# Optimization experiments

Measured on AMD Instinct MI355X. Metric: run time of the kernel, lower is better.

Reference implementation:

```python
import math
import jax, jax.numpy as jnp
import numpy as np

B = 128          # graphs per batch
N = 1024         # nodes per graph
E = 1048576      # total edges (avg degree 8)
F_IN = 64
NHID = 64
NCLS = 10
RATIO = 0.8


def setup_inputs() -> dict:
    key = jax.random.key(0)
    ks = jax.random.split(key, 24)
    x = jax.random.normal(ks[0], (B * N, F_IN), jnp.float32)
    # intra-graph random edges: graph id per edge, local src/dst
    epg = E // B
    gid = jnp.repeat(jnp.arange(B, dtype=jnp.int32), epg)
    src = gid * N + jax.random.randint(ks[1], (E,), 0, N, jnp.int32)
    dst = gid * N + jax.random.randint(ks[2], (E,), 0, N, jnp.int32)
    def lin(k, fi, fo):
        s = 1.0 / np.sqrt(fi)
        return jax.random.uniform(k, (fi, fo), jnp.float32, -s, s)
    p = {
        'W1': lin(ks[3], F_IN, NHID), 'b1': jnp.zeros((NHID,), jnp.float32),
        'Wp1': lin(ks[4], NHID, 1), 'bp1': jnp.zeros((1,), jnp.float32),
        'W2': lin(ks[5], NHID, NHID), 'b2': jnp.zeros((NHID,), jnp.float32),
        'Wp2': lin(ks[6], NHID, 1), 'bp2': jnp.zeros((1,), jnp.float32),
        'W3': lin(ks[7], NHID, NHID), 'b3': jnp.zeros((NHID,), jnp.float32),
        'Wp3': lin(ks[8], NHID, 1), 'bp3': jnp.zeros((1,), jnp.float32),
        'L1w': lin(ks[9], 2 * NHID, NHID), 'L1b': jnp.zeros((NHID,), jnp.float32),
        'L2w': lin(ks[10], NHID, NHID // 2), 'L2b': jnp.zeros((NHID // 2,), jnp.float32),
        'L3w': lin(ks[11], NHID // 2, NCLS), 'L3b': jnp.zeros((NCLS,), jnp.float32),
    }
    return dict(x=x, edge_src=src, edge_dst=dst, **p)


def gcn_conv(x, W, b, src, dst, emask, n):
    # PyG GCNConv: add self loops, symmetric deg normalization
    xw = x @ W
    ew = emask.astype(x.dtype)
    deg = jax.ops.segment_sum(ew, dst, num_segments=n) + 1.0  # +1 self loop
    dis = jax.lax.rsqrt(deg)
    norm = dis[src] * dis[dst] * ew
    agg = jax.ops.segment_sum(xw[src] * norm[:, None], dst, num_segments=n)
    agg = agg + xw * (dis * dis)[:, None]  # self-loop message
    return agg + b


def sag_pool(x, Wp, bp, src, dst, emask, n_cur):
    n_tot = B * n_cur
    k = int(math.ceil(RATIO * n_cur))
    score = gcn_conv(x, Wp, bp, src, dst, emask, n_tot)[:, 0]
    _, idx = jax.lax.top_k(score.reshape(B, n_cur), k)
    perm = (idx + (jnp.arange(B, dtype=jnp.int32) * n_cur)[:, None]).reshape(-1)
    xn = x[perm] * jnp.tanh(score[perm])[:, None]
    new_idx = jnp.full((n_tot,), -1, jnp.int32).at[perm].set(
        jnp.arange(B * k, dtype=jnp.int32))
    ns, nd = new_idx[src], new_idx[dst]
    valid = emask & (ns >= 0) & (nd >= 0)
    return xn, jnp.where(valid, ns, 0), jnp.where(valid, nd, 0), valid, k


def readout(x, k):
    xr = x.reshape(B, k, NHID)
    return jnp.concatenate([xr.max(axis=1), xr.mean(axis=1)], axis=1)


def reference(x, edge_src, edge_dst, W1, b1, Wp1, bp1, W2, b2, Wp2, bp2,
              W3, b3, Wp3, bp3, L1w, L1b, L2w, L2b, L3w, L3b):
    src = edge_src.astype(jnp.int32)
    dst = edge_dst.astype(jnp.int32)
    emask = jnp.ones((E,), bool)
    n = N
    h = jax.nn.relu(gcn_conv(x, W1, b1, src, dst, emask, B * n))
    h, src, dst, emask, n = sag_pool(h, Wp1, bp1, src, dst, emask, n)
    r1 = readout(h, n)
    h = jax.nn.relu(gcn_conv(h, W2, b2, src, dst, emask, B * n))
    h, src, dst, emask, n = sag_pool(h, Wp2, bp2, src, dst, emask, n)
    r2 = readout(h, n)
    h = jax.nn.relu(gcn_conv(h, W3, b3, src, dst, emask, B * n))
    h, src, dst, emask, n = sag_pool(h, Wp3, bp3, src, dst, emask, n)
    r3 = readout(h, n)
    z = r1 + r2 + r3
    z = jax.nn.relu(z @ L1w + L1b)          # dropout is identity in eval
    z = jax.nn.relu(z @ L2w + L2b)
    return jax.nn.log_softmax(z @ L3w + L3b, axis=-1)
```

## Files before the change

kernel.cpp:

```cpp
#include <hip/hip_runtime.h>
#include <math.h>

constexpr int B_  = 128;
constexpr int N_  = 1024;
constexpr int E_  = 1048576;
constexpr int BN_ = B_ * N_;
constexpr int EPG = E_ / B_;
constexpr int NSEG = 16;

typedef short v8s __attribute__((ext_vector_type(8)));
typedef float v4f __attribute__((ext_vector_type(4)));

__device__ __forceinline__ unsigned bf16_rne(unsigned u) {
    return (u + 0x7FFFu + ((u >> 16) & 1u)) >> 16;
}

__global__ __launch_bounds__(1024) void k_csr2(
        const int* __restrict__ src, const int* __restrict__ dst,
        const int* __restrict__ cum,
        int* __restrict__ srt, int* __restrict__ rowptr,
        float* __restrict__ dis, int n) {
    __shared__ int cnt[1024];
    __shared__ int cur[1024];
    __shared__ int cums[1024];
    __shared__ int wsum[17];
    int g = blockIdx.x, tid = threadIdx.x;
    int gb   = g * N_;
    int base = g * n;
    const int eb = g * EPG;

    cums[tid] = cum ? cum[gb + tid] : tid;
    cnt[tid] = 0;
    __syncthreads();
    for (int t = tid; t < EPG; t += 1024) {
        int s = cums[src[eb + t] - gb];
        int d = cums[dst[eb + t] - gb];
        if ((s | d) >= 0) atomicAdd(&cnt[d], 1);
    }
    __syncthreads();

    int c = (tid < n) ? cnt[tid] : 0;
    int v = c;
    int lane = tid & 63, wv = tid >> 6;
    #pragma unroll
    for (int off = 1; off < 64; off <<= 1) {
        int t = __shfl_up(v, off, 64);
        if (lane >= off) v += t;
    }
    if (lane == 63) wsum[wv] = v;
    __syncthreads();
    if (tid == 0) {
        int run = 0;
        #pragma unroll
        for (int i = 0; i < 16; ++i) { int t = wsum[i]; wsum[i] = run; run += t; }
        wsum[16] = run;
    }
    __syncthreads();
    int excl = v - c + wsum[wv];
    if (tid < n) {
        cur[tid] = excl;
        rowptr[g * (n + 1) + tid] = excl;
        dis[base + tid] = rsqrtf((float)c + 1.0f);
    }
    if (tid == 0) rowptr[g * (n + 1) + n] = wsum[16];
    __syncthreads();

    for (int t = tid; t < EPG; t += 1024) {
        int s = cums[src[eb + t] - gb];
        int d = cums[dst[eb + t] - gb];
        if ((s | d) < 0) continue;
        int pos = atomicAdd(&cur[d], 1);
        srt[eb + pos] = s;
    }
}

__global__ __launch_bounds__(1024) void k_wprep3(
        const float* __restrict__ W0, const float* __restrict__ W1,
        const float* __restrict__ W2, unsigned short* __restrict__ wfall) {
    const float* W = (blockIdx.x == 0) ? W0 : (blockIdx.x == 1) ? W1 : W2;
    unsigned short* wf = wfall + (size_t)blockIdx.x * 8192;
    int t = threadIdx.x;
    int l  = t & 63;
    int kk = (t >> 6) & 1;
    int c  = (t >> 7) & 3;
    int p  = (t >> 9) & 1;
    int col = c * 16 + (l & 15);
    int kbase = kk * 32 + (l >> 4) * 8;
    unsigned short o[8];
    #pragma unroll
    for (int j = 0; j < 8; ++j) {
        float w = W[(kbase + j) * 64 + col];
        unsigned u  = __float_as_uint(w);
        unsigned hi = bf16_rne(u);
        if (p == 0) o[j] = (unsigned short)hi;
        else {
            float lo = w - __uint_as_float(hi << 16);
            o[j] = (unsigned short)bf16_rne(__float_as_uint(lo));
        }
    }
    uint4 v;
    v.x = o[0] | ((unsigned)o[1] << 16);
    v.y = o[2] | ((unsigned)o[3] << 16);
    v.z = o[4] | ((unsigned)o[5] << 16);
    v.w = o[6] | ((unsigned)o[7] << 16);
    *reinterpret_cast<uint4*>(wf + (size_t)t * 8) = v;
}

__global__ __launch_bounds__(1024, 8) void k_conv(
        const int* __restrict__ srt, const int* __restrict__ rowptr,
        const float* __restrict__ dis, const float* __restrict__ h,
        const int* __restrict__ perm, const float* __restrict__ ggate,
        const unsigned short* __restrict__ wf,
        const float* __restrict__ bias, const float* __restrict__ Wp,
        float* __restrict__ hout, float* __restrict__ saggq, int n) {
    extern __shared__ float xs[];

    int g = blockIdx.x & 127, q = blockIdx.x >> 7;
    int foff = q * 16;
    int tid  = threadIdx.x;
    int base = g * n;
    const int* grp  = rowptr + g * (n + 1);
    const int* gsrt = srt + g * EPG;

    int lane = tid & 63;
    v8s wh[2], wl[2];
    #pragma unroll
    for (int kk = 0; kk < 2; ++kk) {
        wh[kk] = *reinterpret_cast<const v8s*>(wf + (((size_t)((0*4 + q)*2 + kk))*64 + lane)*8);
        wl[kk] = *reinterpret_cast<const v8s*>(wf + (((size_t)((1*4 + q)*2 + kk))*64 + lane)*8);
    }

    int wave = tid >> 6;
    int m = lane & 15, b = lane >> 4;
    int ntiles = (n + 15) >> 4;
    for (int t = wave; t < ntiles; t += 16) {
        int c0 = t * 16;
        int arow = c0 + m;
        float f[16];
        if (arow < n) {
            float gt = 1.0f;
            size_t r;
            if (perm) { r = (size_t)perm[base + arow]; gt = ggate[base + arow]; }
            else       r = (size_t)(base + arow);
            const float4* hrow = reinterpret_cast<const float4*>(h + r * 64);
            float4 v0 = hrow[b * 2 + 0];
            float4 v1 = hrow[b * 2 + 1];
            float4 v2 = hrow[8 + b * 2 + 0];
            float4 v3 = hrow[8 + b * 2 + 1];
            f[0]=v0.x*gt; f[1]=v0.y*gt; f[2]=v0.z*gt; f[3]=v0.w*gt;
            f[4]=v1.x*gt; f[5]=v1.y*gt; f[6]=v1.z*gt; f[7]=v1.w*gt;
            f[8]=v2.x*gt; f[9]=v2.y*gt; f[10]=v2.z*gt; f[11]=v2.w*gt;
            f[12]=v3.x*gt; f[13]=v3.y*gt; f[14]=v3.z*gt; f[15]=v3.w*gt;
        } else {
            #pragma unroll
            for (int j = 0; j < 16; ++j) f[j] = 0.0f;
        }
        v8s ah[2], al[2];
        #pragma unroll
        for (int ch = 0; ch < 2; ++ch) {
            #pragma unroll
            for (int j = 0; j < 8; ++j) {
                float x = f[ch * 8 + j];
                unsigned u  = __float_as_uint(x);
                unsigned hi = bf16_rne(u);
                float lo = x - __uint_as_float(hi << 16);
                ah[ch][j] = (short)hi;
                al[ch][j] = (short)bf16_rne(__float_as_uint(lo));
            }
        }
        v4f acc = {0.f, 0.f, 0.f, 0.f};
        acc = __builtin_amdgcn_mfma_f32_16x16x32_bf16(ah[0], wh[0], acc, 0, 0, 0);
        acc = __builtin_amdgcn_mfma_f32_16x16x32_bf16(ah[1], wh[1], acc, 0, 0, 0);
        acc = __builtin_amdgcn_mfma_f32_16x16x32_bf16(al[0], wh[0], acc, 0, 0, 0);
        acc = __builtin_amdgcn_mfma_f32_16x16x32_bf16(al[1], wh[1], acc, 0, 0, 0);
        acc = __builtin_amdgcn_mfma_f32_16x16x32_bf16(ah[0], wl[0], acc, 0, 0, 0);
        acc = __builtin_amdgcn_mfma_f32_16x16x32_bf16(ah[1], wl[1], acc, 0, 0, 0);
        acc = __builtin_amdgcn_mfma_f32_16x16x32_bf16(al[0], wl[0], acc, 0, 0, 0);
        acc = __builtin_amdgcn_mfma_f32_16x16x32_bf16(al[1], wl[1], acc, 0, 0, 0);
        #pragma unroll
        for (int reg = 0; reg < 4; ++reg) {
            int orow = c0 + b * 4 + reg;
            if (orow < n) xs[orow * 20 + m] = acc[reg] * dis[base + orow];
        }
    }
    __syncthreads();

    int sub = tid & 3;
    float4 bq  = *reinterpret_cast<const float4*>(bias + foff + sub * 4);
    float4 wp4 = *reinterpret_cast<const float4*>(Wp   + foff + sub * 4);
    for (int row = tid >> 2; row < n; row += 256) {
        int s0 = grp[row], s1 = grp[row + 1];
        float4 acc = *reinterpret_cast<const float4*>(xs + row * 20 + sub * 4);
        for (int j = s0; j < s1; ++j) {
            int s = gsrt[j];
            const float4 v = *reinterpret_cast<const float4*>(xs + s * 20 + sub * 4);
            acc.x += v.x; acc.y += v.y; acc.z += v.z; acc.w += v.w;
        }
        float dsc = dis[base + row];
        float4 o;
        o.x = fmaxf(fmaf(dsc, acc.x, bq.x), 0.0f);
        o.y = fmaxf(fmaf(dsc, acc.y, bq.y), 0.0f);
        o.z = fmaxf(fmaf(dsc, acc.z, bq.z), 0.0f);
        o.w = fmaxf(fmaf(dsc, acc.w, bq.w), 0.0f);
        *reinterpret_cast<float4*>(hout + (size_t)(base + row) * 64 + foff + sub * 4) = o;
        float part = o.x * wp4.x + o.y * wp4.y + o.z * wp4.z + o.w * wp4.w;
        part += __shfl_xor(part, 1, 64);
        part += __shfl_xor(part, 2, 64);
        if (sub == 0) xs[row * 20 + 16] = part * dsc;
    }
    __syncthreads();

    for (int row = tid; row < n; row += 1024) {
        float acc = xs[row * 20 + 16];
        int s1 = grp[row + 1];
        for (int j = grp[row]; j < s1; ++j) acc += xs[gsrt[j] * 20 + 16];
        saggq[(size_t)q * BN_ + base + row] = acc;
    }
}

__global__ __launch_bounds__(1024) void k_score_topk(
        const float* __restrict__ dis, const float* __restrict__ saggq,
        const float* __restrict__ bp, int n, int k,
        int* __restrict__ perm, float* __restrict__ ggate,
        int* __restrict__ cum, int do_compose) {
    __shared__ unsigned long long keys[1024];
    __shared__ int mark[1024];
    int g = blockIdx.x, tid = threadIdx.x;
    int base = g * n;
    float bp0 = bp[0];

    unsigned long long kv = 0ull;
    if (tid < n) {
        float s0 = saggq[0 * (size_t)BN_ + base + tid] + saggq[1 * (size_t)BN_ + base + tid]
                 + saggq[2 * (size_t)BN_ + base + tid] + saggq[3 * (size_t)BN_ + base + tid];
        float sag = dis[base + tid] * s0 + bp0;
        unsigned u  = __float_as_uint(sag);
        unsigned mk = (u & 0x80000000u) ? ~u : (u | 0x80000000u);
        kv = ((unsigned long long)mk << 32) | (unsigned)tid;
    }
    keys[tid] = kv;
    mark[tid] = -1;

    for (int size = 2; size <= 1024; size <<= 1) {
        for (int stride = size >> 1; stride > 0; stride >>= 1) {
            __syncthreads();
            if (tid < 512) {
                int a  = ((tid / stride) * (stride << 1)) + (tid & (stride - 1));
                int bx = a + stride;
                bool asc = ((a & size) == 0);
                unsigned long long ka = keys[a], kb = keys[bx];
                bool sw = asc ? (ka > kb) : (ka < kb);
                if (sw) { keys[a] = kb; keys[bx] = ka; }
            }
        }
    }
    __syncthreads();

    if (tid < k) {
        int j = tid;
        unsigned long long kvv = keys[1023 - j];
        int local   = (int)(kvv & 0xFFFFFFFFull);
        unsigned mk = (unsigned)(kvv >> 32);
        unsigned u  = (mk & 0x80000000u) ? (mk ^ 0x80000000u) : ~mk;
        int newg = g * k + j;
        perm[newg]  = base + local;
        ggate[newg] = tanhf(__uint_as_float(u));
        mark[local] = j;
    }
    __syncthreads();
    if (do_compose) {
        int gb = g * N_;
        int c = (do_compose == 1) ? tid : cum[gb + tid];
        cum[gb + tid] = (c >= 0) ? mark[c] : -1;
    }
}

__global__ __launch_bounds__(256) void k_readout_seg(
        const float* __restrict__ h, const int* __restrict__ perm,
        const float* __restrict__ ggate, int k, float* __restrict__ pz) {
    int g = blockIdx.x / NSEG, seg = blockIdx.x % NSEG;
    int ck = (k + NSEG - 1) / NSEG;
    int j0 = seg * ck;
    int j1 = min(k, j0 + ck);
    __shared__ float gate[64];
    __shared__ int   lperm[64];
    int tid = threadIdx.x;
    for (int j = j0 + tid; j < j1; j += 256) {
        lperm[j - j0] = perm[g * k + j];
        gate[j - j0]  = ggate[g * k + j];
    }
    __syncthreads();
    int lane = tid & 63, w = tid >> 6;
    float mx = -INFINITY, sm = 0.0f;
    for (int j = j0 + w; j < j1; j += 4) {
        float v = h[(size_t)lperm[j - j0] * 64 + lane] * gate[j - j0];
        mx = fmaxf(mx, v); sm += v;
    }
    __shared__ float smx[4][64], ssm[4][64];
    smx[w][lane] = mx; ssm[w][lane] = sm;
    __syncthreads();
    if (w == 0) {
        #pragma unroll
        for (int i = 1; i < 4; ++i) { mx = fmaxf(mx, smx[i][lane]); sm += ssm[i][lane]; }
        float* p = pz + ((size_t)g * NSEG + seg) * 128;
        p[lane]      = mx;
        p[64 + lane] = sm;
    }
}

__global__ __launch_bounds__(128) void k_mlp(const float* __restrict__ pz,
                      const float* __restrict__ L1w, const float* __restrict__ L1b,
                      const float* __restrict__ L2w, const float* __restrict__ L2b,
                      const float* __restrict__ L3w, const float* __restrict__ L3b,
                      float* __restrict__ out) {
    __shared__ float z[128], h1[64], h2[32], lg[10], lse;
    int g = blockIdx.x, tid = threadIdx.x;
    const float kinv[3] = {1.0f / 820.0f, 1.0f / 656.0f, 1.0f / 525.0f};
    float zv = 0.0f;
    if (tid < 64) {
        #pragma unroll
        for (int L = 0; L < 3; ++L) {
            const float* p = pz + (((size_t)L * B_ + g) * NSEG) * 128;
            float mx = -INFINITY;
            #pragma unroll
            for (int s = 0; s < NSEG; ++s) mx = fmaxf(mx, p[s * 128 + tid]);
            zv += mx;
        }
    } else {
        int f = tid - 64;
        #pragma unroll
        for (int L = 0; L < 3; ++L) {
            const float* p = pz + (((size_t)L * B_ + g) * NSEG) * 128;
            float sm = 0.0f;
            #pragma unroll
            for (int s = 0; s < NSEG; ++s) sm += p[s * 128 + 64 + f];
            zv += sm * kinv[L];
        }
    }
    z[tid] = zv;
    __syncthreads();
    if (tid < 64) {
        float acc = L1b[tid];
        for (int i = 0; i < 128; ++i) acc = fmaf(z[i], L1w[i * 64 + tid], acc);
        h1[tid] = fmaxf(acc, 0.0f);
    }
    __syncthreads();
    if (tid < 32) {
        float acc = L2b[tid];
        for (int i = 0; i < 64; ++i) acc = fmaf(h1[i], L2w[i * 32 + tid], acc);
        h2[tid] = fmaxf(acc, 0.0f);
    }
    __syncthreads();
    if (tid < 10) {
        float acc = L3b[tid];
        for (int i = 0; i < 32; ++i) acc = fmaf(h2[i], L3w[i * 10 + tid], acc);
        lg[tid] = acc;
    }
    __syncthreads();
    if (tid == 0) {
        float m = lg[0];
        for (int i = 1; i < 10; ++i) m = fmaxf(m, lg[i]);
        float s = 0.0f;
        for (int i = 0; i < 10; ++i) s += expf(lg[i] - m);
        lse = m + logf(s);
    }
    __syncthreads();
    if (tid < 10) out[g * 10 + tid] = lg[tid] - lse;
}

extern "C" void kernel_launch(void* const* d_in, const int* in_sizes, int n_in,
                              void* d_out, int out_size, void* d_ws, size_t ws_size,
                              hipStream_t stream) {
    const float* x    = (const float*)d_in[0];
    const int*   esrc = (const int*)d_in[1];
    const int*   edst = (const int*)d_in[2];
    const float* W [3] = {(const float*)d_in[3],  (const float*)d_in[7],  (const float*)d_in[11]};
    const float* bb[3] = {(const float*)d_in[4],  (const float*)d_in[8],  (const float*)d_in[12]};
    const float* Wp[3] = {(const float*)d_in[5],  (const float*)d_in[9],  (const float*)d_in[13]};
    const float* bp[3] = {(const float*)d_in[6],  (const float*)d_in[10], (const float*)d_in[14]};
    const float* L1w = (const float*)d_in[15];
    const float* L1b = (const float*)d_in[16];
    const float* L2w = (const float*)d_in[17];
    const float* L2b = (const float*)d_in[18];
    const float* L3w = (const float*)d_in[19];
    const float* L3b = (const float*)d_in[20];
    float* out = (float*)d_out;

    float* fws   = (float*)d_ws;
    float* agg   = fws;
    float* dis   = agg  + (size_t)BN_ * 64;
    float* saggq = dis  + BN_;
    float* ggate = saggq + 4 * (size_t)BN_;
    float* pz    = ggate + BN_;
    int*   perm   = (int*)(pz + 3 * B_ * NSEG * 128);
    int*   cum    = perm + BN_;
    int*   srt    = cum + BN_;
    int*   rowptr = srt + E_;
    unsigned short* wfrag = (unsigned short*)(rowptr + B_ * (N_ + 1));

    hipFuncSetAttribute(reinterpret_cast<const void*>(k_conv),
                        hipFuncAttributeMaxDynamicSharedMemorySize, 20 * 1024 * 4);

    k_wprep3<<<3, 1024, 0, stream>>>(W[0], W[1], W[2], wfrag);

    const int ks_[3] = {820, 656, 525};
    int n = N_;

    for (int L = 0; L < 3; ++L) {
        int k = ks_[L];

        k_csr2<<<B_, 1024, 0, stream>>>(esrc, edst, (L == 0) ? nullptr : cum,
                                        srt, rowptr, dis, n);

        k_conv<<<B_ * 4, 1024, (size_t)(20 * n) * 4, stream>>>(
            srt, rowptr, dis,
            (L == 0) ? x : agg,
            (L == 0) ? nullptr : perm,
            (L == 0) ? nullptr : ggate,
            wfrag + (size_t)L * 8192, bb[L], Wp[L],
            agg, saggq, n);

        k_score_topk<<<B_, 1024, 0, stream>>>(dis, saggq, bp[L], n, k,
                                              perm, ggate, cum, (L < 2) ? (L + 1) : 0);

        k_readout_seg<<<B_ * NSEG, 256, 0, stream>>>(agg, perm, ggate, k,
                                                     pz + (size_t)L * B_ * NSEG * 128);

        n = k;
    }

    k_mlp<<<B_, 128, 0, stream>>>(pz, L1w, L1b, L2w, L2b, L3w, L3b, out);
}
```

Baseline: 247.5 us.

## Sort rows by degree for balanced aggregation and stage CSR in LDS

```diff
diff --git a/kernel.cpp b/kernel.cpp
--- a/kernel.cpp
+++ b/kernel.cpp
@@ -19,10 +19,11 @@
         const int* __restrict__ src, const int* __restrict__ dst,
         const int* __restrict__ cum,
         int* __restrict__ srt, int* __restrict__ rowptr,
-        float* __restrict__ dis, int n) {
+        float* __restrict__ dis, int* __restrict__ rorder, int n) {
     __shared__ int cnt[1024];
     __shared__ int cur[1024];
     __shared__ int cums[1024];
+    __shared__ unsigned skey[1024];
     __shared__ int wsum[17];
     int g = blockIdx.x, tid = threadIdx.x;
     int gb   = g * N_;
@@ -63,7 +64,23 @@
         dis[base + tid] = rsqrtf((float)c + 1.0f);
     }
     if (tid == 0) rowptr[g * (n + 1) + n] = wsum[16];
-    __syncthreads();
+
+    skey[tid] = (tid < n) ? (unsigned)((cnt[tid] << 10) | tid) : 0xFFFFFFFFu;
+    for (int size = 2; size <= 1024; size <<= 1) {
+        for (int stride = size >> 1; stride > 0; stride >>= 1) {
+            __syncthreads();
+            if (tid < 512) {
+                int a  = ((tid / stride) * (stride << 1)) + (tid & (stride - 1));
+                int bx = a + stride;
+                bool asc = ((a & size) == 0);
+                unsigned ka = skey[a], kb = skey[bx];
+                bool sw = asc ? (ka > kb) : (ka < kb);
+                if (sw) { skey[a] = kb; skey[bx] = ka; }
+            }
+        }
+    }
+    __syncthreads();
+    if (tid < n) rorder[base + tid] = (int)(skey[tid] & 1023u);
 
     for (int t = tid; t < EPG; t += 1024) {
         int s = cums[src[eb + t] - gb];
@@ -106,21 +123,27 @@
     *reinterpret_cast<uint4*>(wf + (size_t)t * 8) = v;
 }
 
-__global__ __launch_bounds__(1024, 8) void k_conv(
+__global__ __launch_bounds__(1024, 4) void k_conv(
         const int* __restrict__ srt, const int* __restrict__ rowptr,
+        const int* __restrict__ rorder,
         const float* __restrict__ dis, const float* __restrict__ h,
         const int* __restrict__ perm, const float* __restrict__ ggate,
         const unsigned short* __restrict__ wf,
         const float* __restrict__ bias, const float* __restrict__ Wp,
         float* __restrict__ hout, float* __restrict__ saggq, int n) {
     extern __shared__ float xs[];
+    int* lrp  = (int*)(xs + 20 * n);
+    int* lsrt = lrp + (n + 2);
 
     int g = blockIdx.x & 127, q = blockIdx.x >> 7;
     int foff = q * 16;
     int tid  = threadIdx.x;
     int base = g * n;
-    const int* grp  = rowptr + g * (n + 1);
+
+    for (int i = tid; i <= n; i += 1024) lrp[i] = rowptr[g * (n + 1) + i];
+    int total = rowptr[g * (n + 1) + n];
     const int* gsrt = srt + g * EPG;
+    for (int i = tid; i < total; i += 1024) lsrt[i] = gsrt[i];
 
     int lane = tid & 63;
     v8s wh[2], wl[2];
@@ -188,11 +211,13 @@
     int sub = tid & 3;
     float4 bq  = *reinterpret_cast<const float4*>(bias + foff + sub * 4);
     float4 wp4 = *reinterpret_cast<const float4*>(Wp   + foff + sub * 4);
-    for (int row = tid >> 2; row < n; row += 256) {
-        int s0 = grp[row], s1 = grp[row + 1];
+    const int* rord = rorder + base;
+    for (int i = tid >> 2; i < n; i += 256) {
+        int row = rord[i];
+        int s0 = lrp[row], s1 = lrp[row + 1];
         float4 acc = *reinterpret_cast<const float4*>(xs + row * 20 + sub * 4);
         for (int j = s0; j < s1; ++j) {
-            int s = gsrt[j];
+            int s = lsrt[j];
             const float4 v = *reinterpret_cast<const float4*>(xs + s * 20 + sub * 4);
             acc.x += v.x; acc.y += v.y; acc.z += v.z; acc.w += v.w;
         }
@@ -210,10 +235,11 @@
     }
     __syncthreads();
 
-    for (int row = tid; row < n; row += 1024) {
+    for (int i = tid; i < n; i += 1024) {
+        int row = rord[i];
         float acc = xs[row * 20 + 16];
-        int s1 = grp[row + 1];
-        for (int j = grp[row]; j < s1; ++j) acc += xs[gsrt[j] * 20 + 16];
+        int s1 = lrp[row + 1];
+        for (int j = lrp[row]; j < s1; ++j) acc += xs[lsrt[j] * 20 + 16];
         saggq[(size_t)q * BN_ + base + row] = acc;
     }
 }
@@ -394,12 +420,14 @@
     float* pz    = ggate + BN_;
     int*   perm   = (int*)(pz + 3 * B_ * NSEG * 128);
     int*   cum    = perm + BN_;
-    int*   srt    = cum + BN_;
+    int*   rorder = cum + BN_;
+    int*   srt    = rorder + BN_;
     int*   rowptr = srt + E_;
     unsigned short* wfrag = (unsigned short*)(rowptr + B_ * (N_ + 1));
 
     hipFuncSetAttribute(reinterpret_cast<const void*>(k_conv),
-                        hipFuncAttributeMaxDynamicSharedMemorySize, 20 * 1024 * 4);
+                        hipFuncAttributeMaxDynamicSharedMemorySize,
+                        (21 * 1024 + 2 + EPG) * 4);
 
     k_wprep3<<<3, 1024, 0, stream>>>(W[0], W[1], W[2], wfrag);
 
@@ -410,10 +438,10 @@
         int k = ks_[L];
 
         k_csr2<<<B_, 1024, 0, stream>>>(esrc, edst, (L == 0) ? nullptr : cum,
-                                        srt, rowptr, dis, n);
-
-        k_conv<<<B_ * 4, 1024, (size_t)(20 * n) * 4, stream>>>(
-            srt, rowptr, dis,
+                                        srt, rowptr, dis, rorder, n);
+
+        k_conv<<<B_ * 4, 1024, (size_t)(21 * n + 2 + EPG) * 4, stream>>>(
+            srt, rowptr, rorder, dis,
             (L == 0) ? x : agg,
             (L == 0) ? nullptr : perm,
             (L == 0) ? nullptr : ggate,
```

Result: slower. 313.0 us (+26.5%).
